# Performance work log

Measured on AMD Instinct MI355X. Metric: run time of the kernel, lower is better.

Reference implementation:

```python
import jax, jax.numpy as jnp
import numpy as np

N, E, D_IN, D_OUT = 50000, 800000, 128, 128


def setup_inputs() -> dict:
    key = jax.random.key(0)
    ks = jax.random.split(key, 4)
    x = jax.random.normal(ks[0], (N, D_IN), jnp.float32)
    edge_index = jax.random.randint(ks[1], (2, E), 0, N)
    # GCNConv.lin weight (no bias in lin; bias added after aggregation)
    W = jax.random.normal(ks[2], (D_IN, D_OUT), jnp.float32) / np.sqrt(D_IN)
    b = jnp.zeros((D_OUT,), jnp.float32)
    # edge_weight_predictor: Linear(2*dim_in, 1)
    w_pred = jax.random.normal(ks[3], (2 * D_IN, 1), jnp.float32) / np.sqrt(2 * D_IN)
    b_pred = jnp.zeros((1,), jnp.float32)
    return {"x": x, "edge_index": edge_index, "W": W, "b": b,
            "w_pred": w_pred, "b_pred": b_pred}


def reference(x, edge_index, W, b, w_pred, b_pred):
    n = x.shape[0]
    src, tgt = edge_index[0], edge_index[1]

    # --- learned edge weights: gather, concat, linear, sigmoid ---
    eemb = jnp.concatenate([x[src], x[tgt]], axis=1)          # [E, 2D]
    ew = jax.nn.sigmoid(eemb @ w_pred + b_pred)[:, 0]         # [E]

    # --- GCNConv with edge_weight (PyG gcn_norm: add self-loops w=1) ---
    loop = jnp.arange(n)
    row = jnp.concatenate([src, loop])                        # message sources
    col = jnp.concatenate([tgt, loop])                        # aggregation targets
    w_full = jnp.concatenate([ew, jnp.ones((n,), ew.dtype)])

    deg = jax.ops.segment_sum(w_full, col, num_segments=n)    # weighted in-degree
    dis = jnp.where(deg > 0, jax.lax.rsqrt(deg), 0.0)         # deg^{-1/2}, inf->0
    norm = dis[row] * w_full * dis[col]                       # [E+N]

    xw = x @ W                                                # [N, D_OUT]
    msg = norm[:, None] * xw[row]                             # [E+N, D_OUT]
    out = jax.ops.segment_sum(msg, col, num_segments=n) + b   # [N, D_OUT]
    return out
```

## Files before the change

### kernel.cpp

```cpp
#include <hip/hip_runtime.h>
#include <math.h>

#define D 128
#define NC 32

typedef __attribute__((ext_vector_type(8))) short bf16x8;
typedef __attribute__((ext_vector_type(4))) float f32x4;

__device__ __forceinline__ unsigned int bf16_round(float f) {
  unsigned int u = __float_as_uint(f);
  return (u + 0x7fffu + ((u >> 16) & 1u)) >> 16;
}
__device__ __forceinline__ float bf_lo(unsigned int u) { return __uint_as_float(u << 16); }
__device__ __forceinline__ float bf_hi(unsigned int u) { return __uint_as_float(u & 0xffff0000u); }

__global__ __launch_bounds__(256) void k_pre(const float* __restrict__ x,
                                             const float* __restrict__ w_pred,
                                             const float* __restrict__ W,
                                             const int* __restrict__ tgt,
                                             float* __restrict__ p, float* __restrict__ q,
                                             unsigned int* __restrict__ xbh,
                                             unsigned short* __restrict__ wt,
                                             int* __restrict__ rank,
                                             int* __restrict__ partial,
                                             int n, int E, int nbHist, int total) {
  int bid = blockIdx.x;
  long long h0 = (long long)bid * nbHist / total;
  long long h1 = (long long)(bid + 1) * nbHist / total;
  if (h1 != h0) {
    int e = (int)h0 * 256 + threadIdx.x;
    if (e < E) {
      int t = tgt[e];
      int c = (e >> 8) & (NC - 1);
      rank[e] = atomicAdd(&partial[c * n + t], 1);
    }
    return;
  }
  int pqIdx = bid - (int)h1;
  int ptid = pqIdx * 256 + threadIdx.x;
  if (ptid < 16384) {
    int col = ptid >> 7, k = ptid & 127;
    wt[col * 128 + k] = (unsigned short)bf16_round(W[k * 128 + col]);
  }
  int wid = ptid >> 6;
  int lane = threadIdx.x & 63;
  if (wid >= n) return;
  float2 xv = ((const float2*)(x + (size_t)wid * D))[lane];
  xbh[(size_t)wid * 64 + lane] = bf16_round(xv.x) | (bf16_round(xv.y) << 16);
  float2 wp = ((const float2*)w_pred)[lane];
  float2 wq = ((const float2*)w_pred)[64 + lane];
  float pp = xv.x * wp.x + xv.y * wp.y;
  float qq = xv.x * wq.x + xv.y * wq.y;
#pragma unroll
  for (int off = 32; off > 0; off >>= 1) {
    pp += __shfl_down(pp, off);
    qq += __shfl_down(qq, off);
  }
  if (lane == 0) { p[wid] = pp; q[wid] = qq; }
}

__global__ __launch_bounds__(256) void k_scan1(const int* __restrict__ partial,
                                               int* __restrict__ rowptr,
                                               int* __restrict__ bsum, int n) {
  __shared__ int wsum[4];
  int base = blockIdx.x * 1024 + threadIdx.x * 4;
  int4 v = make_int4(0, 0, 0, 0);
  if (base + 3 < n) {
#pragma unroll
    for (int c = 0; c < NC; ++c) {
      int4 t = *(const int4*)(partial + (size_t)c * n + base);
      v.x += t.x; v.y += t.y; v.z += t.z; v.w += t.w;
    }
  } else {
#pragma unroll
    for (int c = 0; c < NC; ++c) {
      const int* pc = partial + (size_t)c * n;
      if (base + 0 < n) v.x += pc[base + 0];
      if (base + 1 < n) v.y += pc[base + 1];
      if (base + 2 < n) v.z += pc[base + 2];
      if (base + 3 < n) v.w += pc[base + 3];
    }
  }
  int s = v.x + v.y + v.z + v.w;
  int lane = threadIdx.x & 63;
  int wave = threadIdx.x >> 6;
  int incl = s;
#pragma unroll
  for (int off = 1; off < 64; off <<= 1) {
    int t = __shfl_up(incl, off);
    if (lane >= off) incl += t;
  }
  if (lane == 63) wsum[wave] = incl;
  __syncthreads();
  int woff = 0;
#pragma unroll
  for (int w = 0; w < 4; ++w) if (w < wave) woff += wsum[w];
  int excl = woff + incl - s;
  if (base + 0 < n) rowptr[base + 0] = excl;
  if (base + 1 < n) rowptr[base + 1] = excl + v.x;
  if (base + 2 < n) rowptr[base + 2] = excl + v.x + v.y;
  if (base + 3 < n) rowptr[base + 3] = excl + v.x + v.y + v.z;
  if (threadIdx.x == 255) bsum[blockIdx.x] = woff + incl;
}

__global__ __launch_bounds__(256) void k_cursors(int* __restrict__ rowptr,
                                                 const int* __restrict__ bsum,
                                                 const int* __restrict__ partial,
                                                 int* __restrict__ cursor,
                                                 int n, int E, int nb) {
  __shared__ int bpre_s[64];
  if (threadIdx.x < 64) {
    int lane = threadIdx.x;
    int v = (lane < nb) ? bsum[lane] : 0;
    int incl = v;
#pragma unroll
    for (int off = 1; off < 64; off <<= 1) {
      int t = __shfl_up(incl, off);
      if (lane >= off) incl += t;
    }
    bpre_s[lane] = incl - v;
  }
  __syncthreads();
  int t = blockIdx.x * blockDim.x + threadIdx.x;
  if (t < n) {
    int r = rowptr[t] + bpre_s[t >> 10];
    rowptr[t] = r;
#pragma unroll
    for (int c = 0; c < NC; ++c) {
      cursor[c * n + t] = r;
      r += partial[c * n + t];
    }
  }
  if (t == 0) rowptr[n] = E;
}

__global__ __launch_bounds__(256) void k_fg(const int* __restrict__ src,
                                            const int* __restrict__ tgt,
                                            const int* __restrict__ rank,
                                            const int* __restrict__ cursor,
                                            const float* __restrict__ p,
                                            const float* __restrict__ q,
                                            const float* __restrict__ b_pred,
                                            unsigned int* __restrict__ edata,
                                            const short* __restrict__ xbh,
                                            const short* __restrict__ wt,
                                            unsigned int* __restrict__ xwh,
                                            int E, int n, int nbFill, int total) {
  __shared__ float cbuf[4][16 * 128];
  int bid = blockIdx.x;
  long long h0 = (long long)bid * nbFill / total;
  long long h1 = (long long)(bid + 1) * nbFill / total;
  if (h1 != h0) {
    int e = (int)h0 * 256 + threadIdx.x;
    if (e < E) {
      int s = src[e], t = tgt[e];
      int c = (e >> 8) & (NC - 1);
      int pos = cursor[c * n + t] + rank[e];
      float z = p[s] + q[t] + b_pred[0];
      float w = 1.0f / (1.0f + expf(-z));
      edata[pos] = (unsigned int)s | (bf16_round(w) << 16);
    }
    return;
  }
  int gIdx = bid - (int)h1;
  int wave = threadIdx.x >> 6;
  int lane = threadIdx.x & 63;
  int row0 = gIdx * 64 + wave * 16;

  int rA = lane & 15, quad = lane >> 4;
  f32x4 acc[8];
#pragma unroll
  for (int cb = 0; cb < 8; ++cb) acc[cb] = (f32x4){0.f, 0.f, 0.f, 0.f};

  const short* arow = xbh + (size_t)(row0 + rA) * 128 + quad * 8;
  bool arow_ok = (row0 + rA) < n;
#pragma unroll
  for (int kk = 0; kk < 4; ++kk) {
    bf16x8 a;
    if (arow_ok) a = *(const bf16x8*)(arow + kk * 32);
    else a = (bf16x8){0, 0, 0, 0, 0, 0, 0, 0};
#pragma unroll
    for (int cb = 0; cb < 8; ++cb) {
      bf16x8 bf = *(const bf16x8*)(wt + (size_t)(cb * 16 + rA) * 128 + kk * 32 + quad * 8);
      acc[cb] = __builtin_amdgcn_mfma_f32_16x16x32_bf16(a, bf, acc[cb], 0, 0, 0);
    }
  }

#pragma unroll
  for (int cb = 0; cb < 8; ++cb)
#pragma unroll
    for (int r = 0; r < 4; ++r)
      cbuf[wave][(quad * 4 + r) * 128 + cb * 16 + rA] = acc[cb][r];
  __syncthreads();

  int rr = lane >> 2, jj = lane & 3;
  int grow = row0 + rr;
  int ch = jj * 32;
  if (grow < n) {
    const float* cr = &cbuf[wave][rr * 128 + ch];
#pragma unroll
    for (int g = 0; g < 2; ++g) {
      uint4 o;
      o.x = bf16_round(cr[g * 16 + 0])  | (bf16_round(cr[g * 16 + 1]) << 16);
      o.y = bf16_round(cr[g * 16 + 2])  | (bf16_round(cr[g * 16 + 3]) << 16);
      o.z = bf16_round(cr[g * 16 + 4])  | (bf16_round(cr[g * 16 + 5]) << 16);
      o.w = bf16_round(cr[g * 16 + 6])  | (bf16_round(cr[g * 16 + 7]) << 16);
      uint4 o2;
      o2.x = bf16_round(cr[g * 16 + 8])  | (bf16_round(cr[g * 16 + 9]) << 16);
      o2.y = bf16_round(cr[g * 16 + 10]) | (bf16_round(cr[g * 16 + 11]) << 16);
      o2.z = bf16_round(cr[g * 16 + 12]) | (bf16_round(cr[g * 16 + 13]) << 16);
      o2.w = bf16_round(cr[g * 16 + 14]) | (bf16_round(cr[g * 16 + 15]) << 16);
      *(uint4*)(xwh + (size_t)grow * 64 + (ch >> 1) + g * 8)     = o;
      *(uint4*)(xwh + (size_t)grow * 64 + (ch >> 1) + g * 8 + 4) = o2;
    }
  }
}

__global__ __launch_bounds__(256) void k_dis(const int* __restrict__ rowptr,
                                             const unsigned int* __restrict__ edata,
                                             float* __restrict__ dis, int n) {
  int tid = blockIdx.x * 256 + threadIdx.x;
  int grow = tid >> 2;
  int jj = tid & 3;
  if (grow >= n) return;
  int beg = rowptr[grow], end = rowptr[grow + 1];
  float sum = 0.0f;
  for (int j = beg + jj; j < end; j += 4) sum += bf_hi(edata[j]);
  sum += __shfl_xor(sum, 1);
  sum += __shfl_xor(sum, 2);
  if (jj == 0) {
    float d = 1.0f + sum;
    dis[grow] = (d > 0.0f) ? rsqrtf(d) : 0.0f;
  }
}

__global__ __launch_bounds__(256) void k_gather(const int* __restrict__ rowptr,
                                                const unsigned int* __restrict__ edata,
                                                const uint4* __restrict__ xwh4,
                                                const float* __restrict__ dis,
                                                const float* __restrict__ b,
                                                float* __restrict__ out, int n) {
  int wid = (blockIdx.x * blockDim.x + threadIdx.x) >> 6;
  int lane = threadIdx.x & 63;
  if (wid >= n) return;
  int cj = lane & 15;
  int rg = lane >> 4;
  float dt = dis[wid];
  int2 rp = *(const int2*)(rowptr + wid);
  int beg = rp.x, end = rp.y;

  float acc[8];
  if (rg == 0) {
    uint4 v = xwh4[(size_t)wid * 16 + cj];
    acc[0] = dt * bf_lo(v.x); acc[1] = dt * bf_hi(v.x);
    acc[2] = dt * bf_lo(v.y); acc[3] = dt * bf_hi(v.y);
    acc[4] = dt * bf_lo(v.z); acc[5] = dt * bf_hi(v.z);
    acc[6] = dt * bf_lo(v.w); acc[7] = dt * bf_hi(v.w);
  } else {
#pragma unroll
    for (int i = 0; i < 8; ++i) acc[i] = 0.0f;
  }

  for (int j0 = beg; j0 < end; j0 += 64) {
    int m = end - j0; if (m > 64) m = 64;
    unsigned int wl = 0;
    if (lane < m) wl = edata[j0 + lane];
    for (int k = 0; k < m; k += 16) {
      unsigned int w0 = (unsigned int)__shfl((int)wl, k + rg);
      unsigned int w1 = (unsigned int)__shfl((int)wl, k + 4 + rg);
      unsigned int w2 = (unsigned int)__shfl((int)wl, k + 8 + rg);
      unsigned int w3 = (unsigned int)__shfl((int)wl, k + 12 + rg);
      if (k + rg >= m)      w0 = 0;
      if (k + 4 + rg >= m)  w1 = 0;
      if (k + 8 + rg >= m)  w2 = 0;
      if (k + 12 + rg >= m) w3 = 0;
      uint4 v0 = xwh4[(size_t)(w0 & 0xffffu) * 16 + cj];
      uint4 v1 = xwh4[(size_t)(w1 & 0xffffu) * 16 + cj];
      uint4 v2 = xwh4[(size_t)(w2 & 0xffffu) * 16 + cj];
      uint4 v3 = xwh4[(size_t)(w3 & 0xffffu) * 16 + cj];
      float d0 = dis[w0 & 0xffffu];
      float d1 = dis[w1 & 0xffffu];
      float d2 = dis[w2 & 0xffffu];
      float d3 = dis[w3 & 0xffffu];
      float c0 = bf_hi(w0) * d0, c1 = bf_hi(w1) * d1;
      float c2 = bf_hi(w2) * d2, c3 = bf_hi(w3) * d3;
      acc[0] = fmaf(c0, bf_lo(v0.x), acc[0]); acc[1] = fmaf(c0, bf_hi(v0.x), acc[1]);
      acc[2] = fmaf(c0, bf_lo(v0.y), acc[2]); acc[3] = fmaf(c0, bf_hi(v0.y), acc[3]);
      acc[4] = fmaf(c0, bf_lo(v0.z), acc[4]); acc[5] = fmaf(c0, bf_hi(v0.z), acc[5]);
      acc[6] = fmaf(c0, bf_lo(v0.w), acc[6]); acc[7] = fmaf(c0, bf_hi(v0.w), acc[7]);
      acc[0] = fmaf(c1, bf_lo(v1.x), acc[0]); acc[1] = fmaf(c1, bf_hi(v1.x), acc[1]);
      acc[2] = fmaf(c1, bf_lo(v1.y), acc[2]); acc[3] = fmaf(c1, bf_hi(v1.y), acc[3]);
      acc[4] = fmaf(c1, bf_lo(v1.z), acc[4]); acc[5] = fmaf(c1, bf_hi(v1.z), acc[5]);
      acc[6] = fmaf(c1, bf_lo(v1.w), acc[6]); acc[7] = fmaf(c1, bf_hi(v1.w), acc[7]);
      acc[0] = fmaf(c2, bf_lo(v2.x), acc[0]); acc[1] = fmaf(c2, bf_hi(v2.x), acc[1]);
      acc[2] = fmaf(c2, bf_lo(v2.y), acc[2]); acc[3] = fmaf(c2, bf_hi(v2.y), acc[3]);
      acc[4] = fmaf(c2, bf_lo(v2.z), acc[4]); acc[5] = fmaf(c2, bf_hi(v2.z), acc[5]);
      acc[6] = fmaf(c2, bf_lo(v2.w), acc[6]); acc[7] = fmaf(c2, bf_hi(v2.w), acc[7]);
      acc[0] = fmaf(c3, bf_lo(v3.x), acc[0]); acc[1] = fmaf(c3, bf_hi(v3.x), acc[1]);
      acc[2] = fmaf(c3, bf_lo(v3.y), acc[2]); acc[3] = fmaf(c3, bf_hi(v3.y), acc[3]);
      acc[4] = fmaf(c3, bf_lo(v3.z), acc[4]); acc[5] = fmaf(c3, bf_hi(v3.z), acc[5]);
      acc[6] = fmaf(c3, bf_lo(v3.w), acc[6]); acc[7] = fmaf(c3, bf_hi(v3.w), acc[7]);
    }
  }

#pragma unroll
  for (int i = 0; i < 8; ++i) {
    acc[i] += __shfl_xor(acc[i], 16);
    acc[i] += __shfl_xor(acc[i], 32);
  }

  if (rg == 0) {
    float4 b0 = ((const float4*)b)[cj * 2];
    float4 b1 = ((const float4*)b)[cj * 2 + 1];
    float4 o0, o1;
    o0.x = fmaf(dt, acc[0], b0.x); o0.y = fmaf(dt, acc[1], b0.y);
    o0.z = fmaf(dt, acc[2], b0.z); o0.w = fmaf(dt, acc[3], b0.w);
    o1.x = fmaf(dt, acc[4], b1.x); o1.y = fmaf(dt, acc[5], b1.y);
    o1.z = fmaf(dt, acc[6], b1.z); o1.w = fmaf(dt, acc[7], b1.w);
    ((float4*)out)[(size_t)wid * 32 + cj * 2] = o0;
    ((float4*)out)[(size_t)wid * 32 + cj * 2 + 1] = o1;
  }
}

extern "C" void kernel_launch(void* const* d_in, const int* in_sizes, int n_in,
                              void* d_out, int out_size, void* d_ws, size_t ws_size,
                              hipStream_t stream) {
  const float* x      = (const float*)d_in[0];
  const int*   ei     = (const int*)d_in[1];
  const float* W      = (const float*)d_in[2];
  const float* b      = (const float*)d_in[3];
  const float* w_pred = (const float*)d_in[4];
  const float* b_pred = (const float*)d_in[5];

  int n = in_sizes[0] / D;
  int E = in_sizes[1] / 2;
  const int* src = ei;
  const int* tgt = ei + E;

  float* out = (float*)d_out;
  float* ws  = (float*)d_ws;
  unsigned int* xwh = (unsigned int*)ws;
  unsigned int* xbh = xwh + (size_t)n * 64;
  float* p       = (float*)(xbh + (size_t)n * 64);
  float* q       = p + n;
  float* dis     = q + n;
  unsigned int* edata = (unsigned int*)(dis + n);
  int*   rank    = (int*)(edata + E);
  int*   partial = rank + E;
  int*   cursor  = partial + (size_t)NC * n;
  int*   rowptr  = cursor + (size_t)NC * n;
  int*   bsum    = rowptr + n + 1;
  unsigned short* wt = (unsigned short*)(bsum + 64);

  int nb = (n + 1023) / 1024;
  int nbPq = (n + 3) / 4;
  int nbHist = (E + 255) / 256;
  int totalPre = nbPq + nbHist;

  int nbFill = (E + 255) / 256;
  int nbGemm = (n + 63) / 64;
  int totalFg = nbFill + nbGemm;

  (void)hipMemsetAsync(partial, 0, (size_t)NC * n * sizeof(int), stream);
  k_pre<<<totalPre, 256, 0, stream>>>(x, w_pred, W, tgt, p, q, xbh, wt, rank, partial,
                                      n, E, nbHist, totalPre);
  k_scan1<<<nb, 256, 0, stream>>>(partial, rowptr, bsum, n);
  k_cursors<<<(n + 255) / 256, 256, 0, stream>>>(rowptr, bsum, partial, cursor, n, E, nb);
  k_fg<<<totalFg, 256, 0, stream>>>(src, tgt, rank, cursor, p, q, b_pred, edata,
                                    (const short*)xbh, (const short*)wt, xwh,
                                    E, n, nbFill, totalFg);
  k_dis<<<(4 * n + 255) / 256, 256, 0, stream>>>(rowptr, edata, dis, n);
  k_gather<<<(n + 3) / 4, 256, 0, stream>>>(rowptr, edata, (const uint4*)xwh, dis, b, out, n);
}
```

Baseline: 193.1 us.

## Map four rows per wavefront in gather and vectorize edge histogram/fill

The gather kernel now assigns 16 lanes to each destination row, so one wavefront handles four rows. This removes the cross-lane shuffle reduction and the idle lanes on low-degree rows, at the cost of divergence when the four rows have different degrees. The histogram and fill phases now have each thread process four edges with int4 loads, which cuts the block count by four. The GEMM epilogue stages the output through LDS in two halves, halving the shared buffer and dropping the block barrier.

```diff
diff --git a/kernel.cpp b/kernel.cpp
--- a/kernel.cpp
+++ b/kernel.cpp
@@ -13,6 +13,9 @@
 }
 __device__ __forceinline__ float bf_lo(unsigned int u) { return __uint_as_float(u << 16); }
 __device__ __forceinline__ float bf_hi(unsigned int u) { return __uint_as_float(u & 0xffff0000u); }
+__device__ __forceinline__ unsigned int pack2(float a, float b) {
+  return bf16_round(a) | (bf16_round(b) << 16);
+}
 
 __global__ __launch_bounds__(256) void k_pre(const float* __restrict__ x,
                                              const float* __restrict__ w_pred,
@@ -28,11 +31,26 @@
   long long h0 = (long long)bid * nbHist / total;
   long long h1 = (long long)(bid + 1) * nbHist / total;
   if (h1 != h0) {
-    int e = (int)h0 * 256 + threadIdx.x;
-    if (e < E) {
-      int t = tgt[e];
-      int c = (e >> 8) & (NC - 1);
-      rank[e] = atomicAdd(&partial[c * n + t], 1);
+    int e0 = (int)h0 * 1024 + threadIdx.x * 4;
+    if (e0 + 3 < E) {
+      int4 t4 = *(const int4*)(tgt + e0);
+      int c = (e0 >> 8) & (NC - 1);
+      int* pc = partial + (size_t)c * n;
+      int r0 = atomicAdd(&pc[t4.x], 1);
+      int r1 = atomicAdd(&pc[t4.y], 1);
+      int r2 = atomicAdd(&pc[t4.z], 1);
+      int r3 = atomicAdd(&pc[t4.w], 1);
+      *(int4*)(rank + e0) = make_int4(r0, r1, r2, r3);
+    } else {
+#pragma unroll
+      for (int i = 0; i < 4; ++i) {
+        int e = e0 + i;
+        if (e < E) {
+          int t = tgt[e];
+          int c = (e >> 8) & (NC - 1);
+          rank[e] = atomicAdd(&partial[(size_t)c * n + t], 1);
+        }
+      }
     }
     return;
   }
@@ -146,19 +164,48 @@
                                             const short* __restrict__ wt,
                                             unsigned int* __restrict__ xwh,
                                             int E, int n, int nbFill, int total) {
-  __shared__ float cbuf[4][16 * 128];
+  __shared__ float cbuf[4][16 * 64];
   int bid = blockIdx.x;
   long long h0 = (long long)bid * nbFill / total;
   long long h1 = (long long)(bid + 1) * nbFill / total;
   if (h1 != h0) {
-    int e = (int)h0 * 256 + threadIdx.x;
-    if (e < E) {
-      int s = src[e], t = tgt[e];
-      int c = (e >> 8) & (NC - 1);
-      int pos = cursor[c * n + t] + rank[e];
-      float z = p[s] + q[t] + b_pred[0];
-      float w = 1.0f / (1.0f + expf(-z));
-      edata[pos] = (unsigned int)s | (bf16_round(w) << 16);
+    int e0 = (int)h0 * 1024 + threadIdx.x * 4;
+    float bp = b_pred[0];
+    if (e0 + 3 < E) {
+      int4 s4 = *(const int4*)(src + e0);
+      int4 t4 = *(const int4*)(tgt + e0);
+      int4 r4 = *(const int4*)(rank + e0);
+      int c = (e0 >> 8) & (NC - 1);
+      const int* cc = cursor + (size_t)c * n;
+      int pos0 = cc[t4.x] + r4.x;
+      int pos1 = cc[t4.y] + r4.y;
+      int pos2 = cc[t4.z] + r4.z;
+      int pos3 = cc[t4.w] + r4.w;
+      float z0 = p[s4.x] + q[t4.x] + bp;
+      float z1 = p[s4.y] + q[t4.y] + bp;
+      float z2 = p[s4.z] + q[t4.z] + bp;
+      float z3 = p[s4.w] + q[t4.w] + bp;
+      float w0 = 1.0f / (1.0f + expf(-z0));
+      float w1 = 1.0f / (1.0f + expf(-z1));
+      float w2 = 1.0f / (1.0f + expf(-z2));
+      float w3 = 1.0f / (1.0f + expf(-z3));
+      edata[pos0] = (unsigned int)s4.x | (bf16_round(w0) << 16);
+      edata[pos1] = (unsigned int)s4.y | (bf16_round(w1) << 16);
+      edata[pos2] = (unsigned int)s4.z | (bf16_round(w2) << 16);
+      edata[pos3] = (unsigned int)s4.w | (bf16_round(w3) << 16);
+    } else {
+#pragma unroll
+      for (int i = 0; i < 4; ++i) {
+        int e = e0 + i;
+        if (e < E) {
+          int s = src[e], t = tgt[e];
+          int c = (e >> 8) & (NC - 1);
+          int pos = cursor[(size_t)c * n + t] + rank[e];
+          float z = p[s] + q[t] + bp;
+          float w = 1.0f / (1.0f + expf(-z));
+          edata[pos] = (unsigned int)s | (bf16_round(w) << 16);
+        }
+      }
     }
     return;
   }
@@ -186,32 +233,26 @@
     }
   }
 
-#pragma unroll
-  for (int cb = 0; cb < 8; ++cb)
-#pragma unroll
-    for (int r = 0; r < 4; ++r)
-      cbuf[wave][(quad * 4 + r) * 128 + cb * 16 + rA] = acc[cb][r];
-  __syncthreads();
-
   int rr = lane >> 2, jj = lane & 3;
   int grow = row0 + rr;
-  int ch = jj * 32;
-  if (grow < n) {
-    const float* cr = &cbuf[wave][rr * 128 + ch];
-#pragma unroll
-    for (int g = 0; g < 2; ++g) {
-      uint4 o;
-      o.x = bf16_round(cr[g * 16 + 0])  | (bf16_round(cr[g * 16 + 1]) << 16);
-      o.y = bf16_round(cr[g * 16 + 2])  | (bf16_round(cr[g * 16 + 3]) << 16);
-      o.z = bf16_round(cr[g * 16 + 4])  | (bf16_round(cr[g * 16 + 5]) << 16);
-      o.w = bf16_round(cr[g * 16 + 6])  | (bf16_round(cr[g * 16 + 7]) << 16);
-      uint4 o2;
-      o2.x = bf16_round(cr[g * 16 + 8])  | (bf16_round(cr[g * 16 + 9]) << 16);
-      o2.y = bf16_round(cr[g * 16 + 10]) | (bf16_round(cr[g * 16 + 11]) << 16);
-      o2.z = bf16_round(cr[g * 16 + 12]) | (bf16_round(cr[g * 16 + 13]) << 16);
-      o2.w = bf16_round(cr[g * 16 + 14]) | (bf16_round(cr[g * 16 + 15]) << 16);
-      *(uint4*)(xwh + (size_t)grow * 64 + (ch >> 1) + g * 8)     = o;
-      *(uint4*)(xwh + (size_t)grow * 64 + (ch >> 1) + g * 8 + 4) = o2;
+#pragma unroll
+  for (int h = 0; h < 2; ++h) {
+#pragma unroll
+    for (int cb4 = 0; cb4 < 4; ++cb4) {
+      int cb = h * 4 + cb4;
+#pragma unroll
+      for (int r = 0; r < 4; ++r)
+        cbuf[wave][(quad * 4 + r) * 64 + cb4 * 16 + rA] = acc[cb][r];
+    }
+    if (grow < n) {
+      const float* cr = &cbuf[wave][rr * 64 + jj * 16];
+      uint4 o, o2;
+      o.x  = pack2(cr[0],  cr[1]);  o.y  = pack2(cr[2],  cr[3]);
+      o.z  = pack2(cr[4],  cr[5]);  o.w  = pack2(cr[6],  cr[7]);
+      o2.x = pack2(cr[8],  cr[9]);  o2.y = pack2(cr[10], cr[11]);
+      o2.z = pack2(cr[12], cr[13]); o2.w = pack2(cr[14], cr[15]);
+      *(uint4*)(xwh + (size_t)grow * 64 + h * 32 + jj * 8)     = o;
+      *(uint4*)(xwh + (size_t)grow * 64 + h * 32 + jj * 8 + 4) = o2;
     }
   }
 }
@@ -240,18 +281,23 @@
                                                 const float* __restrict__ dis,
                                                 const float* __restrict__ b,
                                                 float* __restrict__ out, int n) {
-  int wid = (blockIdx.x * blockDim.x + threadIdx.x) >> 6;
+  int gw = (blockIdx.x * blockDim.x + threadIdx.x) >> 6;
   int lane = threadIdx.x & 63;
-  if (wid >= n) return;
-  int cj = lane & 15;
-  int rg = lane >> 4;
-  float dt = dis[wid];
-  int2 rp = *(const int2*)(rowptr + wid);
-  int beg = rp.x, end = rp.y;
+  int rg = lane >> 4, cj = lane & 15;
+  int row = gw * 4 + rg;
+  bool valid = row < n;
+
+  float dt = 0.0f;
+  int beg = 0, end = 0;
+  if (valid) {
+    dt = dis[row];
+    int2 rp = *(const int2*)(rowptr + row);
+    beg = rp.x; end = rp.y;
+  }
 
   float acc[8];
-  if (rg == 0) {
-    uint4 v = xwh4[(size_t)wid * 16 + cj];
+  if (valid) {
+    uint4 v = xwh4[(size_t)row * 16 + cj];
     acc[0] = dt * bf_lo(v.x); acc[1] = dt * bf_hi(v.x);
     acc[2] = dt * bf_lo(v.y); acc[3] = dt * bf_hi(v.y);
     acc[4] = dt * bf_lo(v.z); acc[5] = dt * bf_hi(v.z);
@@ -261,19 +307,17 @@
     for (int i = 0; i < 8; ++i) acc[i] = 0.0f;
   }
 
-  for (int j0 = beg; j0 < end; j0 += 64) {
-    int m = end - j0; if (m > 64) m = 64;
-    unsigned int wl = 0;
-    if (lane < m) wl = edata[j0 + lane];
-    for (int k = 0; k < m; k += 16) {
-      unsigned int w0 = (unsigned int)__shfl((int)wl, k + rg);
-      unsigned int w1 = (unsigned int)__shfl((int)wl, k + 4 + rg);
-      unsigned int w2 = (unsigned int)__shfl((int)wl, k + 8 + rg);
-      unsigned int w3 = (unsigned int)__shfl((int)wl, k + 12 + rg);
-      if (k + rg >= m)      w0 = 0;
-      if (k + 4 + rg >= m)  w1 = 0;
-      if (k + 8 + rg >= m)  w2 = 0;
-      if (k + 12 + rg >= m) w3 = 0;
+  for (int j0 = beg; j0 < end; j0 += 16) {
+    int m = end - j0; if (m > 16) m = 16;
+    unsigned int wl = (cj < m) ? edata[j0 + cj] : 0u;
+    for (int k = 0; k < m; k += 4) {
+      unsigned int w0 = (unsigned int)__shfl((int)wl, rg * 16 + k + 0);
+      unsigned int w1 = (unsigned int)__shfl((int)wl, rg * 16 + k + 1);
+      unsigned int w2 = (unsigned int)__shfl((int)wl, rg * 16 + k + 2);
+      unsigned int w3 = (unsigned int)__shfl((int)wl, rg * 16 + k + 3);
+      if (k + 1 >= m) w1 = 0;
+      if (k + 2 >= m) w2 = 0;
+      if (k + 3 >= m) w3 = 0;
       uint4 v0 = xwh4[(size_t)(w0 & 0xffffu) * 16 + cj];
       uint4 v1 = xwh4[(size_t)(w1 & 0xffffu) * 16 + cj];
       uint4 v2 = xwh4[(size_t)(w2 & 0xffffu) * 16 + cj];
@@ -303,13 +347,7 @@
     }
   }
 
-#pragma unroll
-  for (int i = 0; i < 8; ++i) {
-    acc[i] += __shfl_xor(acc[i], 16);
-    acc[i] += __shfl_xor(acc[i], 32);
-  }
-
-  if (rg == 0) {
+  if (valid) {
     float4 b0 = ((const float4*)b)[cj * 2];
     float4 b1 = ((const float4*)b)[cj * 2 + 1];
     float4 o0, o1;
@@ -317,8 +355,8 @@
     o0.z = fmaf(dt, acc[2], b0.z); o0.w = fmaf(dt, acc[3], b0.w);
     o1.x = fmaf(dt, acc[4], b1.x); o1.y = fmaf(dt, acc[5], b1.y);
     o1.z = fmaf(dt, acc[6], b1.z); o1.w = fmaf(dt, acc[7], b1.w);
-    ((float4*)out)[(size_t)wid * 32 + cj * 2] = o0;
-    ((float4*)out)[(size_t)wid * 32 + cj * 2 + 1] = o1;
+    ((float4*)out)[(size_t)row * 32 + cj * 2] = o0;
+    ((float4*)out)[(size_t)row * 32 + cj * 2 + 1] = o1;
   }
 }
 
@@ -354,12 +392,15 @@
 
   int nb = (n + 1023) / 1024;
   int nbPq = (n + 3) / 4;
-  int nbHist = (E + 255) / 256;
+  int nbHist = (E + 1023) / 1024;
   int totalPre = nbPq + nbHist;
 
-  int nbFill = (E + 255) / 256;
+  int nbFill = (E + 1023) / 1024;
   int nbGemm = (n + 63) / 64;
   int totalFg = nbFill + nbGemm;
+
+  int wavesG = (n + 3) / 4;
+  int nbGather = (wavesG + 3) / 4;
 
   (void)hipMemsetAsync(partial, 0, (size_t)NC * n * sizeof(int), stream);
   k_pre<<<totalPre, 256, 0, stream>>>(x, w_pred, W, tgt, p, q, xbh, wt, rank, partial,
@@ -370,5 +411,5 @@
                                     (const short*)xbh, (const short*)wt, xwh,
                                     E, n, nbFill, totalFg);
   k_dis<<<(4 * n + 255) / 256, 256, 0, stream>>>(rowptr, edata, dis, n);
-  k_gather<<<(n + 3) / 4, 256, 0, stream>>>(rowptr, edata, (const uint4*)xwh, dis, b, out, n);
-}
+  k_gather<<<nbGather, 256, 0, stream>>>(rowptr, edata, (const uint4*)xwh, dis, b, out, n);
+}
```

New measurement: 190.2 us (median of 2 runs). No clear change (-1.5%).
